# Performance work log

Measured on AMD Instinct MI355X. Metric: run time of the kernel, lower is better.

The kernel has to match this reference:

```python
import jax, jax.numpy as jnp
import numpy as np

B, N, K = 4, 4096, 10   # batch, num points, ED_nsample
SA, ED = 128, 4          # SA_conv_out, ED_conv_out


def _bn_pack(key, C):
    # rows: gamma, beta, running_mean, running_var (eval-mode BatchNorm1d)
    kg, kb, km, kv = jax.random.split(key, 4)
    g = 1.0 + 0.1 * jax.random.normal(kg, (C,))
    b = 0.1 * jax.random.normal(kb, (C,))
    m = 0.1 * jax.random.normal(km, (C,))
    v = jax.random.uniform(kv, (C,), minval=0.5, maxval=1.5)
    return jnp.stack([g, b, m, v])


def _conv_params(key, o, c):
    kw, kb = jax.random.split(key)
    return (jax.random.normal(kw, (o, c)) * (1.0 / np.sqrt(c)),
            0.01 * jax.random.normal(kb, (o,)))


def setup_inputs() -> dict:
    key = jax.random.key(0)
    ks = iter(jax.random.split(key, 32))
    inp = {}
    inp['pointcloud'] = jax.random.normal(next(ks), (B, N, 3), dtype=jnp.float32)
    inp['h1'] = jax.random.normal(next(ks), (B, SA, N), dtype=jnp.float32)      # Pointnet_Backbone output
    inp['h2'] = jax.random.normal(next(ks), (B, 1024, N), dtype=jnp.float32)    # DGCNN output
    shapes = {'dg1': (256, 1024), 'dg2': (64, 256), 'dg3': (32, 64),
              'c1': (512, 160), 'c2': (256, 512), 'c3': (128, 256), 'f': (128, 132)}
    for name, (o, c) in shapes.items():
        W, b = _conv_params(next(ks), o, c)
        inp['W_' + name], inp['b_' + name] = W, b
        inp['bn_' + name] = _bn_pack(next(ks), o)
    inp['W_ed1'] = jax.random.normal(next(ks), (ED, 3)) * 0.5
    inp['b_ed1'] = 0.01 * jax.random.normal(next(ks), (ED,))
    inp['W_ed2'] = jax.random.normal(next(ks), (ED, ED)) * 0.5
    inp['b_ed2'] = 0.01 * jax.random.normal(next(ks), (ED,))
    inp['numpoints'] = N
    return inp


def _bn1d(x, p, eps=1e-5):
    # x: [B, C, N]; p rows: gamma, beta, mean, var
    g, b, m, v = p
    inv = g * jax.lax.rsqrt(v + eps)
    return x * inv[:, None] + (b - m * inv)[:, None]


def _conv1(x, W, b):
    # 1x1 Conv1d == channel matmul. x: [B,C,N], W: [O,C]
    return jnp.einsum('oc,bcn->bon', W, x) + b[:, None]


def reference(pointcloud, h1, h2,
              W_dg1, b_dg1, bn_dg1, W_dg2, b_dg2, bn_dg2, W_dg3, b_dg3, bn_dg3,
              W_c1, b_c1, bn_c1, W_c2, b_c2, bn_c2, W_c3, b_c3, bn_c3,
              W_f, b_f, bn_f, W_ed1, b_ed1, W_ed2, b_ed2, numpoints):
    relu = jax.nn.relu
    xyz = pointcloud[..., :3]  # [B,N,3]

    # DGCNN feature reduction: 1024 -> 256 -> 64 -> 32
    h2_ = relu(_bn1d(_conv1(h2, W_dg1, b_dg1), bn_dg1))
    h2_ = relu(_bn1d(_conv1(h2_, W_dg2, b_dg2), bn_dg2))
    h2_ = relu(_bn1d(_conv1(h2_, W_dg3, b_dg3), bn_dg3))

    # fused feature: 160 -> 512 -> 256 -> 128
    f = jnp.concatenate([h1, h2_], axis=1)
    f_ = relu(_bn1d(_conv1(f, W_c1, b_c1), bn_c1))
    f_ = relu(_bn1d(_conv1(f_, W_c2, b_c2), bn_c2))
    f_ = relu(_bn1d(_conv1(f_, W_c3, b_c3), bn_c3))

    # knn_point: K nearest neighbors of each point within its cloud
    sq = jnp.sum(xyz * xyz, axis=-1)  # [B,N]
    d = sq[:, :, None] + sq[:, None, :] - 2.0 * jnp.einsum('bnd,bmd->bnm', xyz, xyz)
    _, idx = jax.lax.top_k(-d, K)  # [B,N,K]
    nbr = jax.vmap(lambda p, i: p[i])(xyz, idx)  # [B,N,K,3]

    # per-point 3x3 covariance + eigenvalues
    c = nbr - jnp.mean(nbr, axis=2, keepdims=True)
    cov = jnp.einsum('bnki,bnkj->bnij', c, c) / K  # [B,N,3,3]
    ev = jnp.linalg.eigvalsh(cov)  # [B,N,3] ascending

    # sub3_ED: Linear(3,4) -> ReLU -> Linear(4,4)
    ef = relu(ev @ W_ed1.T + b_ed1) @ W_ed2.T + b_ed2  # [B,N,4]
    ef_t = ef.transpose(0, 2, 1)  # [B,4,N]

    z = jnp.concatenate([f_, ef_t], axis=1)  # [B,132,N]
    z_ = relu(_bn1d(_conv1(z, W_f, b_f), bn_f))  # [B,128,N]
    return (xyz, z_, h1, h2_, ef_t)
```

## Files before the change

### kernel.cpp

```cpp
#include <hip/hip_runtime.h>
#include <hip/hip_bf16.h>
#include <math.h>

typedef __hip_bfloat16 bf16;

#define BB 4
#define NN 4096
#define KNB 10
#define KQ 16
#define KS 16
#define KC (NN / KS)

typedef __bf16 bfv8 __attribute__((ext_vector_type(8)));
typedef float  f32x4 __attribute__((ext_vector_type(4)));

__device__ __forceinline__ float ldT(const float* p) { return *p; }
__device__ __forceinline__ float ldT(const bf16* p)  { return __bfloat162float(*p); }
__device__ __forceinline__ void  stT(float* p, float v) { *p = v; }
__device__ __forceinline__ void  stT(bf16* p,  float v) { *p = __float2bfloat16(v); }

__device__ __forceinline__ unsigned short f2us(float x) {
  union { bf16 h; unsigned short u; } cv;
  cv.h = __float2bfloat16(x);
  return cv.u;
}

__device__ __forceinline__ void ld8bits(const float* p, unsigned short* s) {
  const float4 a = *(const float4*)p;
  const float4 b = *(const float4*)(p + 4);
  s[0] = f2us(a.x); s[1] = f2us(a.y); s[2] = f2us(a.z); s[3] = f2us(a.w);
  s[4] = f2us(b.x); s[5] = f2us(b.y); s[6] = f2us(b.z); s[7] = f2us(b.w);
}
__device__ __forceinline__ void ld8bits(const bf16* p, unsigned short* s) {
  const uint2 a = *(const uint2*)p;
  const uint2 b = *(const uint2*)(p + 4);
  s[0] = a.x & 0xffff; s[1] = a.x >> 16; s[2] = a.y & 0xffff; s[3] = a.y >> 16;
  s[4] = b.x & 0xffff; s[5] = b.x >> 16; s[6] = b.y & 0xffff; s[7] = b.y >> 16;
}

__device__ __forceinline__ bfv8 ldfrag(const unsigned short* p) {
  union { uint4 u; bfv8 v; } t;
  t.u = *(const uint4*)p;
  return t.v;
}

__global__ void k_sniff(const unsigned int* __restrict__ pcw, int* __restrict__ flag) {
  if (blockIdx.x == 0 && threadIdx.x == 0) {
    int hits = 0;
    for (int i = 0; i < 64; ++i) {
      unsigned int e = (pcw[i] >> 7) & 0xFF;
      if (e >= 100 && e <= 140) ++hits;
    }
    *flag = (hits >= 40) ? 1 : 0;
  }
}

template <class TI, class TO>
__global__ void k_prep(const int* __restrict__ flag, int want,
                       const TI* __restrict__ pc, float* __restrict__ xyz,
                       TO* __restrict__ out0) {
  if (*flag != want) return;
  int i = blockIdx.x * blockDim.x + threadIdx.x;
  if (i >= BB * NN) return;
  float x = ldT(pc + i * 3 + 0), y = ldT(pc + i * 3 + 1), z = ldT(pc + i * 3 + 2);
  xyz[i * 3 + 0] = x; xyz[i * 3 + 1] = y; xyz[i * 3 + 2] = z;
  stT(out0 + i * 3 + 0, x); stT(out0 + i * 3 + 1, y); stT(out0 + i * 3 + 2, z);
}

template <class TI, class TO>
__global__ void k_h1(const int* __restrict__ flag, int want,
                     const TI* __restrict__ h1, TO* __restrict__ out2,
                     bf16* __restrict__ fbuf) {
  if (*flag != want) return;
  int i = blockIdx.x * blockDim.x + threadIdx.x;
  const int per = 128 * NN;
  if (i >= BB * per) return;
  float v = ldT(h1 + i);
  stT(out2 + i, v);
  int b = i / per, r = i - b * per;
  fbuf[(size_t)b * 160 * NN + r] = __float2bfloat16(v);
}

__global__ __launch_bounds__(256) void k_knn(const float* __restrict__ xyz,
                                             int* __restrict__ idxout) {
  __shared__ float md[KS * KNB][KQ];
  __shared__ int   mi[KS * KNB][KQ];
  const int tid = threadIdx.x;
  const int q = tid & (KQ - 1);
  const int s = tid >> 4;
  const int n = blockIdx.x * KQ + q;
  const int b = blockIdx.y;
  const float* xb = xyz + (size_t)b * NN * 3;
  const float xn = xb[n * 3 + 0];
  const float yn = xb[n * 3 + 1];
  const float zn = xb[n * 3 + 2];
  const float sn = xn * xn + yn * yn + zn * zn;

  float dk[KNB]; int ik[KNB];
  #pragma unroll
  for (int t = 0; t < KNB; ++t) { dk[t] = 1e30f; ik[t] = NN; }

  const float* cp = xb + s * KC * 3;
  for (int j = 0; j < KC; ++j) {
    float xm = cp[j * 3 + 0];
    float ym = cp[j * 3 + 1];
    float zm = cp[j * 3 + 2];
    float sm = fmaf(xm, xm, fmaf(ym, ym, zm * zm));
    float dot = fmaf(xn, xm, fmaf(yn, ym, zn * zm));
    float dist = (sn + sm) - 2.0f * dot;
    if (dist < dk[KNB - 1]) {
      dk[KNB - 1] = dist; ik[KNB - 1] = s * KC + j;
      #pragma unroll
      for (int t = KNB - 1; t > 0; --t) {
        if (dk[t] < dk[t - 1]) {
          float td = dk[t]; dk[t] = dk[t - 1]; dk[t - 1] = td;
          int ti = ik[t]; ik[t] = ik[t - 1]; ik[t - 1] = ti;
        }
      }
    }
  }
  #pragma unroll
  for (int t = 0; t < KNB; ++t) { md[s * KNB + t][q] = dk[t]; mi[s * KNB + t][q] = ik[t]; }
  __syncthreads();
  if (s == 0) {
    int head[KS];
    #pragma unroll
    for (int t = 0; t < KS; ++t) head[t] = 0;
    int* op = idxout + ((size_t)b * NN + n) * KNB;
    for (int r = 0; r < KNB; ++r) {
      float best = 1e31f; int bi = NN; int bs = 0;
      #pragma unroll
      for (int t = 0; t < KS; ++t) {
        float v = md[t * KNB + head[t]][q];
        int vi  = mi[t * KNB + head[t]][q];
        if (v < best || (v == best && vi < bi)) { best = v; bi = vi; bs = t; }
      }
      op[r] = bi; ++head[bs];
    }
  }
}

template <class TP, class TO>
__global__ void k_ef(const int* __restrict__ flag, int want,
                     const float* __restrict__ xyz, const int* __restrict__ idxin,
                     const TP* __restrict__ W1, const TP* __restrict__ b1,
                     const TP* __restrict__ W2, const TP* __restrict__ b2,
                     TO* __restrict__ out4, bf16* __restrict__ zbuf) {
  if (*flag != want) return;
  int i = blockIdx.x * blockDim.x + threadIdx.x;
  if (i >= BB * NN) return;
  int b = i / NN, n = i - b * NN;
  const float* xb = xyz + (size_t)b * NN * 3;
  const int* id = idxin + (size_t)i * KNB;
  double px[KNB], py[KNB], pz[KNB];
  double mx = 0, my = 0, mz = 0;
  #pragma unroll
  for (int k = 0; k < KNB; ++k) {
    int j = id[k];
    px[k] = (double)xb[j * 3 + 0];
    py[k] = (double)xb[j * 3 + 1];
    pz[k] = (double)xb[j * 3 + 2];
    mx += px[k]; my += py[k]; mz += pz[k];
  }
  mx /= KNB; my /= KNB; mz /= KNB;
  double c00 = 0, c01 = 0, c02 = 0, c11 = 0, c12 = 0, c22 = 0;
  #pragma unroll
  for (int k = 0; k < KNB; ++k) {
    double dx = px[k] - mx, dy = py[k] - my, dz = pz[k] - mz;
    c00 += dx * dx; c01 += dx * dy; c02 += dx * dz;
    c11 += dy * dy; c12 += dy * dz; c22 += dz * dz;
  }
  c00 /= KNB; c01 /= KNB; c02 /= KNB; c11 /= KNB; c12 /= KNB; c22 /= KNB;
  double e0, e1, e2;
  {
    double p1 = c01 * c01 + c02 * c02 + c12 * c12;
    double q = (c00 + c11 + c22) / 3.0;
    double d0 = c00 - q, d1 = c11 - q, d2 = c22 - q;
    double p2 = d0 * d0 + d1 * d1 + d2 * d2 + 2.0 * p1;
    if (p2 <= 0.0) {
      e0 = e1 = e2 = q;
    } else {
      double p = sqrt(p2 / 6.0);
      double ip = 1.0 / p;
      double b00 = d0 * ip, b11 = d1 * ip, b22 = d2 * ip;
      double b01 = c01 * ip, b02 = c02 * ip, b12 = c12 * ip;
      double det = b00 * (b11 * b22 - b12 * b12)
                 - b01 * (b01 * b22 - b12 * b02)
                 + b02 * (b01 * b12 - b11 * b02);
      double r = 0.5 * det;
      r = fmin(1.0, fmax(-1.0, r));
      double phi = acos(r) / 3.0;
      double lmax = q + 2.0 * p * cos(phi);
      double lmin = q + 2.0 * p * cos(phi + 2.0943951023931953);
      e0 = lmin; e2 = lmax; e1 = 3.0 * q - lmax - lmin;
    }
  }
  float ev0 = (float)e0, ev1 = (float)e1, ev2 = (float)e2;
  float h[4];
  #pragma unroll
  for (int o = 0; o < 4; ++o) {
    float t = ev0 * ldT(W1 + o * 3 + 0) + ev1 * ldT(W1 + o * 3 + 1)
            + ev2 * ldT(W1 + o * 3 + 2) + ldT(b1 + o);
    h[o] = fmaxf(t, 0.f);
  }
  #pragma unroll
  for (int j = 0; j < 4; ++j) {
    float t = h[0] * ldT(W2 + j * 4 + 0) + h[1] * ldT(W2 + j * 4 + 1)
            + h[2] * ldT(W2 + j * 4 + 2) + h[3] * ldT(W2 + j * 4 + 3)
            + ldT(b2 + j);
    stT(out4 + ((size_t)b * 4 + j) * NN + n, t);
    zbuf[((size_t)b * 132 + 128 + j) * NN + n] = __float2bfloat16(t);
  }
}

template <class TX, class TP, class TO>
__global__ __launch_bounds__(256) void k_gemm(
    const int* __restrict__ flag, int want,
    const TX* __restrict__ X, int C,
    const TP* __restrict__ W, const TP* __restrict__ bias,
    const TP* __restrict__ bn, int O,
    TO* __restrict__ Yout, int YRo, int yoffo,
    bf16* __restrict__ Ybuf, int YRb, int yoffb) {
  if (*flag != want) return;
  __shared__ __align__(16) unsigned short Ws[64][72];
  __shared__ __align__(16) unsigned short Xs[64][72];
  const int tid  = threadIdx.x;
  const int lane = tid & 63;
  const int wv   = tid >> 6;
  const int wr = wv >> 1, wc = wv & 1;
  const int l15 = lane & 15, lg = lane >> 4;
  const int nBase = blockIdx.x * 64;
  const int oBase = blockIdx.y * 64;
  const int b = blockIdx.z;
  const TX* Xb = X + (size_t)b * C * NN;

  f32x4 acc[2][2];
  #pragma unroll
  for (int m = 0; m < 2; ++m)
    #pragma unroll
    for (int n = 0; n < 2; ++n) acc[m][n] = (f32x4){0.f, 0.f, 0.f, 0.f};

  const int wo  = tid >> 3;
  const int wc0 = (tid & 7) << 3;
  const int xc  = tid >> 3;
  const int xn0 = (tid & 7) << 3;

  for (int cb = 0; cb < C; cb += 64) {
    #pragma unroll
    for (int h = 0; h < 2; ++h) {
      const int o  = wo + h * 32;
      const int go = oBase + o, gc = cb + wc0;
      const int crem = C - gc;
      unsigned short s[8];
      if (go < O && crem >= 8) {
        ld8bits(W + (size_t)go * C + gc, s);
      } else {
        #pragma unroll
        for (int j = 0; j < 8; ++j)
          s[j] = (go < O && j < crem) ? f2us(ldT(W + (size_t)go * C + gc + j))
                                      : (unsigned short)0;
      }
      uint4 u;
      u.x = (unsigned)s[0] | ((unsigned)s[1] << 16);
      u.y = (unsigned)s[2] | ((unsigned)s[3] << 16);
      u.z = (unsigned)s[4] | ((unsigned)s[5] << 16);
      u.w = (unsigned)s[6] | ((unsigned)s[7] << 16);
      *(uint4*)&Ws[o][wc0] = u;
    }
    #pragma unroll
    for (int h = 0; h < 2; ++h) {
      const int c  = xc + h * 32;
      const int gc = cb + c;
      unsigned short s[8];
      if (gc < C) {
        ld8bits(Xb + (size_t)gc * NN + nBase + xn0, s);
      } else {
        #pragma unroll
        for (int j = 0; j < 8; ++j) s[j] = 0;
      }
      const int xcol = c ^ xn0;
      #pragma unroll
      for (int j = 0; j < 8; ++j) Xs[xn0 + j][xcol] = s[j];
    }
    __syncthreads();
    #pragma unroll
    for (int kk = 0; kk < 2; ++kk) {
      bfv8 af[2], xf[2];
      #pragma unroll
      for (int m = 0; m < 2; ++m)
        af[m] = ldfrag(&Ws[wr * 32 + m * 16 + l15][kk * 32 + lg * 8]);
      #pragma unroll
      for (int n = 0; n < 2; ++n) {
        const int nl  = wc * 32 + n * 16 + l15;
        const int col = (kk * 32 + lg * 8) ^ (((nl >> 3) & 7) << 3);
        xf[n] = ldfrag(&Xs[nl][col]);
      }
      #pragma unroll
      for (int m = 0; m < 2; ++m)
        #pragma unroll
        for (int n = 0; n < 2; ++n)
          acc[m][n] = __builtin_amdgcn_mfma_f32_16x16x32_bf16(af[m], xf[n], acc[m][n], 0, 0, 0);
    }
    __syncthreads();
  }

  #pragma unroll
  for (int m = 0; m < 2; ++m) {
    const int ob = oBase + wr * 32 + m * 16 + lg * 4;
    #pragma unroll
    for (int r = 0; r < 4; ++r) {
      const int oo = ob + r;
      if (oo >= O) continue;
      const float bc  = ldT(bias + oo);
      const float g   = ldT(bn + oo);
      const float bbv = ldT(bn + O + oo);
      const float mm  = ldT(bn + 2 * O + oo);
      const float vv  = ldT(bn + 3 * O + oo);
      const float inv = g / sqrtf(vv + 1e-5f);
      const float sh  = bbv - mm * inv;
      #pragma unroll
      for (int n = 0; n < 2; ++n) {
        const int nn2 = nBase + wc * 32 + n * 16 + l15;
        const float rv = fmaxf((acc[m][n][r] + bc) * inv + sh, 0.f);
        if (Yout) stT(Yout + ((size_t)b * YRo + yoffo + oo) * NN + nn2, rv);
        if (Ybuf) Ybuf[((size_t)b * YRb + yoffb + oo) * NN + nn2] = __float2bfloat16(rv);
      }
    }
  }
}

template <class TI>
static void launch_prep(int want, const int* flag, void* const* d_in, void* d_out,
                        hipStream_t stream, float* xyz) {
  typedef TI TO;
  const TI* pc = (const TI*)d_in[0];
  TO* out0 = (TO*)d_out;
  k_prep<TI, TO><<<dim3((BB * NN + 255) / 256), 256, 0, stream>>>(flag, want, pc, xyz, out0);
}

template <class TI>
static void launch_rest(int want, const int* flag,
                        void* const* d_in, void* d_out, hipStream_t stream,
                        float* xyz, int* idx,
                        bf16* t512, bf16* t256, bf16* t64, bf16* fbuf, bf16* zbuf) {
  typedef TI TO;
  const TI* h1    = (const TI*)d_in[1];
  const TI* h2    = (const TI*)d_in[2];
  const TI* W_dg1 = (const TI*)d_in[3];  const TI* b_dg1 = (const TI*)d_in[4];  const TI* bn_dg1 = (const TI*)d_in[5];
  const TI* W_dg2 = (const TI*)d_in[6];  const TI* b_dg2 = (const TI*)d_in[7];  const TI* bn_dg2 = (const TI*)d_in[8];
  const TI* W_dg3 = (const TI*)d_in[9];  const TI* b_dg3 = (const TI*)d_in[10]; const TI* bn_dg3 = (const TI*)d_in[11];
  const TI* W_c1  = (const TI*)d_in[12]; const TI* b_c1  = (const TI*)d_in[13]; const TI* bn_c1  = (const TI*)d_in[14];
  const TI* W_c2  = (const TI*)d_in[15]; const TI* b_c2  = (const TI*)d_in[16]; const TI* bn_c2  = (const TI*)d_in[17];
  const TI* W_c3  = (const TI*)d_in[18]; const TI* b_c3  = (const TI*)d_in[19]; const TI* bn_c3  = (const TI*)d_in[20];
  const TI* W_f   = (const TI*)d_in[21]; const TI* b_f   = (const TI*)d_in[22]; const TI* bn_f   = (const TI*)d_in[23];
  const TI* W_ed1 = (const TI*)d_in[24]; const TI* b_ed1 = (const TI*)d_in[25];
  const TI* W_ed2 = (const TI*)d_in[26]; const TI* b_ed2 = (const TI*)d_in[27];

  TO* out  = (TO*)d_out;
  TO* out1 = out + 49152;
  TO* out2 = out1 + 2097152;
  TO* out3 = out2 + 2097152;
  TO* out4 = out3 + 524288;

  dim3 blk(256);
  k_h1<TI, TO><<<dim3((BB * 128 * NN + 255) / 256), 256, 0, stream>>>(flag, want, h1, out2, fbuf);
  k_gemm<TI, TI, TO><<<dim3(64, 4, BB), blk, 0, stream>>>(flag, want, h2, 1024, W_dg1, b_dg1, bn_dg1, 256,
                                                          (TO*)nullptr, 0, 0, t256, 256, 0);
  k_gemm<bf16, TI, TO><<<dim3(64, 1, BB), blk, 0, stream>>>(flag, want, t256, 256, W_dg2, b_dg2, bn_dg2, 64,
                                                            (TO*)nullptr, 0, 0, t64, 64, 0);
  k_gemm<bf16, TI, TO><<<dim3(64, 1, BB), blk, 0, stream>>>(flag, want, t64, 64, W_dg3, b_dg3, bn_dg3, 32,
                                                            out3, 32, 0, fbuf, 160, 128);
  k_gemm<bf16, TI, TO><<<dim3(64, 8, BB), blk, 0, stream>>>(flag, want, fbuf, 160, W_c1, b_c1, bn_c1, 512,
                                                            (TO*)nullptr, 0, 0, t512, 512, 0);
  k_ef<TI, TO><<<dim3((BB * NN + 255) / 256), 256, 0, stream>>>(flag, want, xyz, idx, W_ed1, b_ed1, W_ed2, b_ed2, out4, zbuf);
  k_gemm<bf16, TI, TO><<<dim3(64, 4, BB), blk, 0, stream>>>(flag, want, t512, 512, W_c2, b_c2, bn_c2, 256,
                                                            (TO*)nullptr, 0, 0, t256, 256, 0);
  k_gemm<bf16, TI, TO><<<dim3(64, 2, BB), blk, 0, stream>>>(flag, want, t256, 256, W_c3, b_c3, bn_c3, 128,
                                                            (TO*)nullptr, 0, 0, zbuf, 132, 0);
  k_gemm<bf16, TI, TO><<<dim3(64, 2, BB), blk, 0, stream>>>(flag, want, zbuf, 132, W_f, b_f, bn_f, 128,
                                                            out1, 128, 0, (bf16*)nullptr, 0, 0);
}

extern "C" void kernel_launch(void* const* d_in, const int* in_sizes, int n_in,
                              void* d_out, int out_size, void* d_ws, size_t ws_size,
                              hipStream_t stream) {
  char* ws = (char*)d_ws;
  int*    flag = (int*)(ws + 0);
  float*  xyz  = (float*)(ws + 1024);
  int*    idx  = (int*)(ws + 328704);
  bf16*   t512 = (bf16*)(ws + 1048576);
  bf16*   t256 = (bf16*)(ws + 17825792);
  bf16*   t64  = (bf16*)(ws + 26214400);
  bf16*   fbuf = (bf16*)(ws + 28311552);
  bf16*   zbuf = (bf16*)(ws + 33554432);

  k_sniff<<<1, 64, 0, stream>>>((const unsigned int*)d_in[0], flag);

  launch_prep<float>(0, flag, d_in, d_out, stream, xyz);
  launch_prep<bf16>(1, flag, d_in, d_out, stream, xyz);

  k_knn<<<dim3(NN / KQ, BB), 256, 0, stream>>>(xyz, idx);

  launch_rest<float>(0, flag, d_in, d_out, stream, xyz, idx, t512, t256, t64, fbuf, zbuf);
  launch_rest<bf16>(1, flag, d_in, d_out, stream, xyz, idx, t512, t256, t64, fbuf, zbuf);
}
```

Measured before the change: 442.2 us.

## Replace per-thread insertion kNN with block-wide radix histogram selection

```diff
diff --git a/kernel.cpp b/kernel.cpp
--- a/kernel.cpp
+++ b/kernel.cpp
@@ -7,9 +7,7 @@
 #define BB 4
 #define NN 4096
 #define KNB 10
-#define KQ 16
-#define KS 16
-#define KC (NN / KS)
+#define KNQ 4
 
 typedef __bf16 bfv8 __attribute__((ext_vector_type(8)));
 typedef float  f32x4 __attribute__((ext_vector_type(4)));
@@ -59,7 +57,7 @@
 __global__ void k_prep(const int* __restrict__ flag, int want,
                        const TI* __restrict__ pc, float* __restrict__ xyz,
                        TO* __restrict__ out0) {
-  if (*flag != want) return;
+  if (flag && *flag != want) return;
   int i = blockIdx.x * blockDim.x + threadIdx.x;
   if (i >= BB * NN) return;
   float x = ldT(pc + i * 3 + 0), y = ldT(pc + i * 3 + 1), z = ldT(pc + i * 3 + 2);
@@ -71,7 +69,7 @@
 __global__ void k_h1(const int* __restrict__ flag, int want,
                      const TI* __restrict__ h1, TO* __restrict__ out2,
                      bf16* __restrict__ fbuf) {
-  if (*flag != want) return;
+  if (flag && *flag != want) return;
   int i = blockIdx.x * blockDim.x + threadIdx.x;
   const int per = 128 * NN;
   if (i >= BB * per) return;
@@ -81,61 +79,137 @@
   fbuf[(size_t)b * 160 * NN + r] = __float2bfloat16(v);
 }
 
-__global__ __launch_bounds__(256) void k_knn(const float* __restrict__ xyz,
-                                             int* __restrict__ idxout) {
-  __shared__ float md[KS * KNB][KQ];
-  __shared__ int   mi[KS * KNB][KQ];
+template <int BPT>
+__device__ __forceinline__ void hist_pick(unsigned int* hist, unsigned int* spart,
+                                          unsigned int* sexcl,
+                                          unsigned int* selt, unsigned int* selless,
+                                          unsigned int R, int tid) {
+  unsigned int s = 0;
+  #pragma unroll
+  for (int k = 0; k < BPT; ++k) s += hist[tid * BPT + k];
+  spart[tid] = s;
+  __syncthreads();
+  if (tid < 64) {
+    const unsigned int a0 = spart[tid*4+0], a1 = spart[tid*4+1];
+    const unsigned int a2 = spart[tid*4+2], a3 = spart[tid*4+3];
+    const unsigned int c = a0 + a1 + a2 + a3;
+    unsigned int inc = c;
+    #pragma unroll
+    for (int off = 1; off < 64; off <<= 1) {
+      const unsigned int t = __shfl_up(inc, off, 64);
+      if (tid >= off) inc += t;
+    }
+    unsigned int run = inc - c;
+    sexcl[tid*4+0] = run; run += a0;
+    sexcl[tid*4+1] = run; run += a1;
+    sexcl[tid*4+2] = run; run += a2;
+    sexcl[tid*4+3] = run;
+  }
+  __syncthreads();
+  unsigned int cum = sexcl[tid];
+  #pragma unroll
+  for (int k = 0; k < BPT; ++k) {
+    const unsigned int h = hist[tid * BPT + k];
+    const unsigned int nc = cum + h;
+    if (cum < R && R <= nc) { *selt = (unsigned)(tid * BPT + k); *selless = cum; }
+    cum = nc;
+  }
+  __syncthreads();
+}
+
+__global__ __launch_bounds__(256, 4) void k_knn(const float* __restrict__ xyz,
+                                                int* __restrict__ idxout) {
+  __shared__ unsigned int hist[2048];
+  __shared__ unsigned int spart[256];
+  __shared__ unsigned int sexcl[256];
+  __shared__ unsigned int sel_t, sel_less, s_cnt1, s_found;
+  __shared__ unsigned int wmin[4];
   const int tid = threadIdx.x;
-  const int q = tid & (KQ - 1);
-  const int s = tid >> 4;
-  const int n = blockIdx.x * KQ + q;
   const int b = blockIdx.y;
+  const int nBase = blockIdx.x * KNQ;
   const float* xb = xyz + (size_t)b * NN * 3;
-  const float xn = xb[n * 3 + 0];
-  const float yn = xb[n * 3 + 1];
-  const float zn = xb[n * 3 + 2];
-  const float sn = xn * xn + yn * yn + zn * zn;
-
-  float dk[KNB]; int ik[KNB];
-  #pragma unroll
-  for (int t = 0; t < KNB; ++t) { dk[t] = 1e30f; ik[t] = NN; }
-
-  const float* cp = xb + s * KC * 3;
-  for (int j = 0; j < KC; ++j) {
-    float xm = cp[j * 3 + 0];
-    float ym = cp[j * 3 + 1];
-    float zm = cp[j * 3 + 2];
-    float sm = fmaf(xm, xm, fmaf(ym, ym, zm * zm));
-    float dot = fmaf(xn, xm, fmaf(yn, ym, zn * zm));
-    float dist = (sn + sm) - 2.0f * dot;
-    if (dist < dk[KNB - 1]) {
-      dk[KNB - 1] = dist; ik[KNB - 1] = s * KC + j;
-      #pragma unroll
-      for (int t = KNB - 1; t > 0; --t) {
-        if (dk[t] < dk[t - 1]) {
-          float td = dk[t]; dk[t] = dk[t - 1]; dk[t - 1] = td;
-          int ti = ik[t]; ik[t] = ik[t - 1]; ik[t - 1] = ti;
-        }
-      }
-    }
-  }
-  #pragma unroll
-  for (int t = 0; t < KNB; ++t) { md[s * KNB + t][q] = dk[t]; mi[s * KNB + t][q] = ik[t]; }
-  __syncthreads();
-  if (s == 0) {
-    int head[KS];
-    #pragma unroll
-    for (int t = 0; t < KS; ++t) head[t] = 0;
+
+  float cx[16], cy[16], cz[16], cn[16];
+  #pragma unroll
+  for (int i = 0; i < 16; ++i) {
+    const int j = i * 256 + tid;
+    cx[i] = xb[j * 3 + 0]; cy[i] = xb[j * 3 + 1]; cz[i] = xb[j * 3 + 2];
+    cn[i] = fmaf(cx[i], cx[i], fmaf(cy[i], cy[i], cz[i] * cz[i]));
+  }
+
+  for (int qq = 0; qq < KNQ; ++qq) {
+    const int n = nBase + qq;
+    const float xn = xb[n * 3 + 0], yn = xb[n * 3 + 1], zn = xb[n * 3 + 2];
+    const float sn = fmaf(xn, xn, fmaf(yn, yn, zn * zn));
+    unsigned int key[16];
+    #pragma unroll
+    for (int i = 0; i < 16; ++i) {
+      const float dot = fmaf(xn, cx[i], fmaf(yn, cy[i], zn * cz[i]));
+      const float d = (sn + cn[i]) - 2.0f * dot;
+      const unsigned int u = __float_as_uint(d);
+      key[i] = ((int)u < 0) ? ~u : (u | 0x80000000u);
+    }
+    __syncthreads();
+    #pragma unroll
+    for (int k = 0; k < 8; ++k) hist[tid * 8 + k] = 0u;
+    __syncthreads();
+    #pragma unroll
+    for (int i = 0; i < 16; ++i) atomicAdd(&hist[key[i] >> 21], 1u);
+    __syncthreads();
+    hist_pick<8>(hist, spart, sexcl, &sel_t, &sel_less, KNB, tid);
+    const unsigned int t0 = sel_t;
+    const unsigned int r1 = KNB - sel_less;
+    #pragma unroll
+    for (int k = 0; k < 8; ++k) hist[tid * 8 + k] = 0u;
+    __syncthreads();
+    #pragma unroll
+    for (int i = 0; i < 16; ++i)
+      if ((key[i] >> 21) == t0) atomicAdd(&hist[(key[i] >> 10) & 2047u], 1u);
+    __syncthreads();
+    hist_pick<8>(hist, spart, sexcl, &sel_t, &sel_less, r1, tid);
+    const unsigned int t1 = sel_t;
+    const unsigned int r2 = r1 - sel_less;
+    const unsigned int p22 = (t0 << 11) | t1;
+    #pragma unroll
+    for (int k = 0; k < 4; ++k) hist[tid * 4 + k] = 0u;
+    __syncthreads();
+    #pragma unroll
+    for (int i = 0; i < 16; ++i)
+      if ((key[i] >> 10) == p22) atomicAdd(&hist[key[i] & 1023u], 1u);
+    __syncthreads();
+    hist_pick<4>(hist, spart, sexcl, &sel_t, &sel_less, r2, tid);
+    const unsigned int T = (p22 << 10) | sel_t;
+    if (tid == 0) s_cnt1 = 0u;
+    __syncthreads();
     int* op = idxout + ((size_t)b * NN + n) * KNB;
-    for (int r = 0; r < KNB; ++r) {
-      float best = 1e31f; int bi = NN; int bs = 0;
-      #pragma unroll
-      for (int t = 0; t < KS; ++t) {
-        float v = md[t * KNB + head[t]][q];
-        int vi  = mi[t * KNB + head[t]][q];
-        if (v < best || (v == best && vi < bi)) { best = v; bi = vi; bs = t; }
-      }
-      op[r] = bi; ++head[bs];
+    #pragma unroll
+    for (int i = 0; i < 16; ++i) {
+      if (key[i] < T) {
+        const unsigned int pos = atomicAdd(&s_cnt1, 1u);
+        op[pos] = i * 256 + tid;
+      }
+    }
+    __syncthreads();
+    const unsigned int cnt1 = s_cnt1;
+    int prev = -1;
+    for (unsigned int r = cnt1; r < KNB; ++r) {
+      int local = 0x7fffffff;
+      #pragma unroll
+      for (int i = 0; i < 16; ++i) {
+        const int j = i * 256 + tid;
+        if (key[i] == T && j > prev) local = min(local, j);
+      }
+      #pragma unroll
+      for (int off = 32; off > 0; off >>= 1) local = min(local, __shfl_xor(local, off, 64));
+      if ((tid & 63) == 0) wmin[tid >> 6] = (unsigned)local;
+      __syncthreads();
+      if (tid == 0) {
+        const unsigned int m = min(min(wmin[0], wmin[1]), min(wmin[2], wmin[3]));
+        s_found = m;
+        op[r] = (int)m;
+      }
+      __syncthreads();
+      prev = (int)s_found;
     }
   }
 }
@@ -146,7 +220,7 @@
                      const TP* __restrict__ W1, const TP* __restrict__ b1,
                      const TP* __restrict__ W2, const TP* __restrict__ b2,
                      TO* __restrict__ out4, bf16* __restrict__ zbuf) {
-  if (*flag != want) return;
+  if (flag && *flag != want) return;
   int i = blockIdx.x * blockDim.x + threadIdx.x;
   if (i >= BB * NN) return;
   int b = i / NN, n = i - b * NN;
@@ -221,7 +295,7 @@
     const TP* __restrict__ bn, int O,
     TO* __restrict__ Yout, int YRo, int yoffo,
     bf16* __restrict__ Ybuf, int YRb, int yoffb) {
-  if (*flag != want) return;
+  if (flag && *flag != want) return;
   __shared__ __align__(16) unsigned short Ws[64][72];
   __shared__ __align__(16) unsigned short Xs[64][72];
   const int tid  = threadIdx.x;
@@ -394,13 +468,26 @@
   bf16*   fbuf = (bf16*)(ws + 28311552);
   bf16*   zbuf = (bf16*)(ws + 33554432);
 
-  k_sniff<<<1, 64, 0, stream>>>((const unsigned int*)d_in[0], flag);
-
-  launch_prep<float>(0, flag, d_in, d_out, stream, xyz);
-  launch_prep<bf16>(1, flag, d_in, d_out, stream, xyz);
-
-  k_knn<<<dim3(NN / KQ, BB), 256, 0, stream>>>(xyz, idx);
-
-  launch_rest<float>(0, flag, d_in, d_out, stream, xyz, idx, t512, t256, t64, fbuf, zbuf);
-  launch_rest<bf16>(1, flag, d_in, d_out, stream, xyz, idx, t512, t256, t64, fbuf, zbuf);
-}
+  int mode = -1;
+  if (in_sizes) {
+    if (in_sizes[0] == (int)(BB * NN * 3 * sizeof(float))) mode = 0;
+    else if (in_sizes[0] == (int)(BB * NN * 3 * sizeof(bf16))) mode = 1;
+  }
+
+  if (mode < 0) {
+    k_sniff<<<1, 64, 0, stream>>>((const unsigned int*)d_in[0], flag);
+    launch_prep<float>(0, flag, d_in, d_out, stream, xyz);
+    launch_prep<bf16>(1, flag, d_in, d_out, stream, xyz);
+  } else if (mode == 0) {
+    launch_prep<float>(0, nullptr, d_in, d_out, stream, xyz);
+  } else {
+    launch_prep<bf16>(1, nullptr, d_in, d_out, stream, xyz);
+  }
+
+  k_knn<<<dim3(NN / KNQ, BB), 256, 0, stream>>>(xyz, idx);
+
+  if (mode != 1) launch_rest<float>(0, mode < 0 ? flag : nullptr, d_in, d_out, stream,
+                                    xyz, idx, t512, t256, t64, fbuf, zbuf);
+  if (mode != 0) launch_rest<bf16>(1, mode < 0 ? flag : nullptr, d_in, d_out, stream,
+                                   xyz, idx, t512, t256, t64, fbuf, zbuf);
+}
```

After: 479.4 us. +8.4%, slower.

## Use threshold-filtered two-pass KNN and pick dtype path on host

Applied to the files above, without the earlier changes.

```diff
diff --git a/kernel.cpp b/kernel.cpp
--- a/kernel.cpp
+++ b/kernel.cpp
@@ -10,6 +10,7 @@
 #define KQ 16
 #define KS 16
 #define KC (NN / KS)
+#define KCAP 128
 
 typedef __bf16 bfv8 __attribute__((ext_vector_type(8)));
 typedef float  f32x4 __attribute__((ext_vector_type(4)));
@@ -59,7 +60,7 @@
 __global__ void k_prep(const int* __restrict__ flag, int want,
                        const TI* __restrict__ pc, float* __restrict__ xyz,
                        TO* __restrict__ out0) {
-  if (*flag != want) return;
+  if (flag && *flag != want) return;
   int i = blockIdx.x * blockDim.x + threadIdx.x;
   if (i >= BB * NN) return;
   float x = ldT(pc + i * 3 + 0), y = ldT(pc + i * 3 + 1), z = ldT(pc + i * 3 + 2);
@@ -71,7 +72,7 @@
 __global__ void k_h1(const int* __restrict__ flag, int want,
                      const TI* __restrict__ h1, TO* __restrict__ out2,
                      bf16* __restrict__ fbuf) {
-  if (*flag != want) return;
+  if (flag && *flag != want) return;
   int i = blockIdx.x * blockDim.x + threadIdx.x;
   const int per = 128 * NN;
   if (i >= BB * per) return;
@@ -83,8 +84,11 @@
 
 __global__ __launch_bounds__(256) void k_knn(const float* __restrict__ xyz,
                                              int* __restrict__ idxout) {
-  __shared__ float md[KS * KNB][KQ];
-  __shared__ int   mi[KS * KNB][KQ];
+  __shared__ float sminb[KS][KQ];
+  __shared__ float stau[KQ];
+  __shared__ float sd[KQ][KCAP];
+  __shared__ int   si[KQ][KCAP];
+  __shared__ unsigned int scnt[KQ];
   const int tid = threadIdx.x;
   const int q = tid & (KQ - 1);
   const int s = tid >> 4;
@@ -94,49 +98,109 @@
   const float xn = xb[n * 3 + 0];
   const float yn = xb[n * 3 + 1];
   const float zn = xb[n * 3 + 2];
-  const float sn = xn * xn + yn * yn + zn * zn;
-
-  float dk[KNB]; int ik[KNB];
-  #pragma unroll
-  for (int t = 0; t < KNB; ++t) { dk[t] = 1e30f; ik[t] = NN; }
+  const float sn = fmaf(xn, xn, fmaf(yn, yn, zn * zn));
+  if (tid < KQ) scnt[tid] = 0u;
 
   const float* cp = xb + s * KC * 3;
+  float mv0 = 1e30f, mv1 = 1e30f, mv2 = 1e30f, mv3 = 1e30f;
+  for (int j = 0; j < KC; j += 4) {
+    #pragma unroll
+    for (int u = 0; u < 4; ++u) {
+      const float xm = cp[(j + u) * 3 + 0];
+      const float ym = cp[(j + u) * 3 + 1];
+      const float zm = cp[(j + u) * 3 + 2];
+      const float sm = fmaf(xm, xm, fmaf(ym, ym, zm * zm));
+      const float dot = fmaf(xn, xm, fmaf(yn, ym, zn * zm));
+      const float d = (sn + sm) - 2.0f * dot;
+      if (u == 0) mv0 = fminf(mv0, d);
+      else if (u == 1) mv1 = fminf(mv1, d);
+      else if (u == 2) mv2 = fminf(mv2, d);
+      else mv3 = fminf(mv3, d);
+    }
+  }
+  sminb[s][q] = fminf(fminf(mv0, mv1), fminf(mv2, mv3));
+  __syncthreads();
+
+  if (tid < KQ) {
+    float arr[KNB];
+    #pragma unroll
+    for (int t = 0; t < KNB; ++t) arr[t] = 1e30f;
+    #pragma unroll
+    for (int ss = 0; ss < KS; ++ss) {
+      const float v = sminb[ss][tid];
+      if (v < arr[KNB - 1]) {
+        arr[KNB - 1] = v;
+        #pragma unroll
+        for (int t = KNB - 1; t > 0; --t)
+          if (arr[t] < arr[t - 1]) { const float tm = arr[t]; arr[t] = arr[t - 1]; arr[t - 1] = tm; }
+      }
+    }
+    stau[tid] = arr[KNB - 1];
+  }
+  __syncthreads();
+  const float tau = stau[q];
+
   for (int j = 0; j < KC; ++j) {
-    float xm = cp[j * 3 + 0];
-    float ym = cp[j * 3 + 1];
-    float zm = cp[j * 3 + 2];
-    float sm = fmaf(xm, xm, fmaf(ym, ym, zm * zm));
-    float dot = fmaf(xn, xm, fmaf(yn, ym, zn * zm));
-    float dist = (sn + sm) - 2.0f * dot;
-    if (dist < dk[KNB - 1]) {
-      dk[KNB - 1] = dist; ik[KNB - 1] = s * KC + j;
-      #pragma unroll
-      for (int t = KNB - 1; t > 0; --t) {
-        if (dk[t] < dk[t - 1]) {
-          float td = dk[t]; dk[t] = dk[t - 1]; dk[t - 1] = td;
-          int ti = ik[t]; ik[t] = ik[t - 1]; ik[t - 1] = ti;
+    const float xm = cp[j * 3 + 0];
+    const float ym = cp[j * 3 + 1];
+    const float zm = cp[j * 3 + 2];
+    const float sm = fmaf(xm, xm, fmaf(ym, ym, zm * zm));
+    const float dot = fmaf(xn, xm, fmaf(yn, ym, zn * zm));
+    const float d = (sn + sm) - 2.0f * dot;
+    if (d <= tau) {
+      const unsigned int pos = atomicAdd(&scnt[q], 1u);
+      if (pos < KCAP) { sd[q][pos] = d; si[q][pos] = s * KC + j; }
+    }
+  }
+  __syncthreads();
+
+  if (tid < KQ) {
+    const int qq = tid;
+    const int nq = blockIdx.x * KQ + qq;
+    int* op = idxout + ((size_t)b * NN + nq) * KNB;
+    const unsigned int m = scnt[qq];
+    float dk[KNB]; int ik[KNB];
+    #pragma unroll
+    for (int t = 0; t < KNB; ++t) { dk[t] = 1e30f; ik[t] = NN; }
+    if (m <= KCAP) {
+      for (unsigned int e = 0; e < m; ++e) {
+        const float d = sd[qq][e];
+        const int j = si[qq][e];
+        if (d < dk[KNB - 1] || (d == dk[KNB - 1] && j < ik[KNB - 1])) {
+          dk[KNB - 1] = d; ik[KNB - 1] = j;
+          #pragma unroll
+          for (int t = KNB - 1; t > 0; --t) {
+            if (dk[t] < dk[t - 1] || (dk[t] == dk[t - 1] && ik[t] < ik[t - 1])) {
+              const float td = dk[t]; dk[t] = dk[t - 1]; dk[t - 1] = td;
+              const int ti = ik[t]; ik[t] = ik[t - 1]; ik[t - 1] = ti;
+            }
+          }
         }
       }
-    }
-  }
-  #pragma unroll
-  for (int t = 0; t < KNB; ++t) { md[s * KNB + t][q] = dk[t]; mi[s * KNB + t][q] = ik[t]; }
-  __syncthreads();
-  if (s == 0) {
-    int head[KS];
-    #pragma unroll
-    for (int t = 0; t < KS; ++t) head[t] = 0;
-    int* op = idxout + ((size_t)b * NN + n) * KNB;
-    for (int r = 0; r < KNB; ++r) {
-      float best = 1e31f; int bi = NN; int bs = 0;
-      #pragma unroll
-      for (int t = 0; t < KS; ++t) {
-        float v = md[t * KNB + head[t]][q];
-        int vi  = mi[t * KNB + head[t]][q];
-        if (v < best || (v == best && vi < bi)) { best = v; bi = vi; bs = t; }
-      }
-      op[r] = bi; ++head[bs];
-    }
+    } else {
+      const float xq = xb[nq * 3 + 0], yq = xb[nq * 3 + 1], zq = xb[nq * 3 + 2];
+      const float sq = fmaf(xq, xq, fmaf(yq, yq, zq * zq));
+      for (int j = 0; j < NN; ++j) {
+        const float xm = xb[j * 3 + 0];
+        const float ym = xb[j * 3 + 1];
+        const float zm = xb[j * 3 + 2];
+        const float sm = fmaf(xm, xm, fmaf(ym, ym, zm * zm));
+        const float dot = fmaf(xq, xm, fmaf(yq, ym, zq * zm));
+        const float d = (sq + sm) - 2.0f * dot;
+        if (d < dk[KNB - 1] || (d == dk[KNB - 1] && j < ik[KNB - 1])) {
+          dk[KNB - 1] = d; ik[KNB - 1] = j;
+          #pragma unroll
+          for (int t = KNB - 1; t > 0; --t) {
+            if (dk[t] < dk[t - 1] || (dk[t] == dk[t - 1] && ik[t] < ik[t - 1])) {
+              const float td = dk[t]; dk[t] = dk[t - 1]; dk[t - 1] = td;
+              const int ti = ik[t]; ik[t] = ik[t - 1]; ik[t - 1] = ti;
+            }
+          }
+        }
+      }
+    }
+    #pragma unroll
+    for (int t = 0; t < KNB; ++t) op[t] = ik[t];
   }
 }
 
@@ -146,7 +210,7 @@
                      const TP* __restrict__ W1, const TP* __restrict__ b1,
                      const TP* __restrict__ W2, const TP* __restrict__ b2,
                      TO* __restrict__ out4, bf16* __restrict__ zbuf) {
-  if (*flag != want) return;
+  if (flag && *flag != want) return;
   int i = blockIdx.x * blockDim.x + threadIdx.x;
   if (i >= BB * NN) return;
   int b = i / NN, n = i - b * NN;
@@ -221,7 +285,7 @@
     const TP* __restrict__ bn, int O,
     TO* __restrict__ Yout, int YRo, int yoffo,
     bf16* __restrict__ Ybuf, int YRb, int yoffb) {
-  if (*flag != want) return;
+  if (flag && *flag != want) return;
   __shared__ __align__(16) unsigned short Ws[64][72];
   __shared__ __align__(16) unsigned short Xs[64][72];
   const int tid  = threadIdx.x;
@@ -394,13 +458,26 @@
   bf16*   fbuf = (bf16*)(ws + 28311552);
   bf16*   zbuf = (bf16*)(ws + 33554432);
 
-  k_sniff<<<1, 64, 0, stream>>>((const unsigned int*)d_in[0], flag);
-
-  launch_prep<float>(0, flag, d_in, d_out, stream, xyz);
-  launch_prep<bf16>(1, flag, d_in, d_out, stream, xyz);
+  int mode = -1;
+  if (in_sizes) {
+    if (in_sizes[0] == (int)(BB * NN * 3 * sizeof(float))) mode = 0;
+    else if (in_sizes[0] == (int)(BB * NN * 3 * sizeof(bf16))) mode = 1;
+  }
+
+  if (mode < 0) {
+    k_sniff<<<1, 64, 0, stream>>>((const unsigned int*)d_in[0], flag);
+    launch_prep<float>(0, flag, d_in, d_out, stream, xyz);
+    launch_prep<bf16>(1, flag, d_in, d_out, stream, xyz);
+  } else if (mode == 0) {
+    launch_prep<float>(0, nullptr, d_in, d_out, stream, xyz);
+  } else {
+    launch_prep<bf16>(1, nullptr, d_in, d_out, stream, xyz);
+  }
 
   k_knn<<<dim3(NN / KQ, BB), 256, 0, stream>>>(xyz, idx);
 
-  launch_rest<float>(0, flag, d_in, d_out, stream, xyz, idx, t512, t256, t64, fbuf, zbuf);
-  launch_rest<bf16>(1, flag, d_in, d_out, stream, xyz, idx, t512, t256, t64, fbuf, zbuf);
-}
+  if (mode != 1) launch_rest<float>(0, mode < 0 ? flag : nullptr, d_in, d_out, stream,
+                                    xyz, idx, t512, t256, t64, fbuf, zbuf);
+  if (mode != 0) launch_rest<bf16>(1, mode < 0 ? flag : nullptr, d_in, d_out, stream,
+                                   xyz, idx, t512, t256, t64, fbuf, zbuf);
+}
```

After: 406.7 us. 8.0% less time.
